# Optimization experiments

Hardware: AMD Instinct MI355X
Metric: run time of the kernel (lower is better)

The kernel has to match this reference:

```python
import jax, jax.numpy as jnp
import numpy as np

S, B, D_DEC, D_ALIGN, D_ENC = 1024, 64, 1024, 1024, 1024


def setup_inputs() -> dict:
    key = jax.random.key(0)
    ks = jax.random.split(key, 6)
    scale = 1.0 / np.sqrt(D_DEC)
    return {
        "s_tm1": jax.random.normal(ks[0], (B, D_DEC), jnp.float32),
        "xs_h": jax.random.normal(ks[1], (S, B, D_ENC), jnp.float32),
        "uh": jax.random.normal(ks[2], (S, B, D_ALIGN), jnp.float32),
        "xs_mask": jnp.ones((S, B), jnp.float32),
        "sa_w": jax.random.normal(ks[3], (D_ALIGN, D_DEC), jnp.float32) * scale,
        "sa_b": jnp.zeros((D_ALIGN,), jnp.float32),
        "a1_w": jax.random.normal(ks[4], (1, D_ALIGN), jnp.float32) * scale,
        "a1_b": jnp.zeros((1,), jnp.float32),
    }


def reference(s_tm1, xs_h, uh, xs_mask, sa_w, sa_b, a1_w, a1_b):
    # sa(s_tm1): [B, align]
    sa_s = s_tm1 @ sa_w.T + sa_b
    # broadcast-add over seq dim, tanh, then a1 (align -> 1), squeeze -> [S, B]
    h = jnp.tanh(sa_s[None, :, :] + uh)                  # [S, B, align]
    e = jnp.einsum('sba,a->sb', h, a1_w[0]) + a1_b[0]    # [S, B]
    # masked softmax over dim 0 (seq)
    ex = jnp.exp(e - jnp.max(e, axis=0, keepdims=True))
    ex = ex * xs_mask
    e_ij = ex / jnp.sum(ex, axis=0, keepdims=True)       # [S, B]
    # weighted sum over seq: [B, D_enc]
    attend = jnp.einsum('sb,sbd->bd', e_ij, xs_h)
    return (e_ij, attend)
```

## Files before the change

kernel.cpp:

```cpp
#include <hip/hip_runtime.h>
#include <hip/hip_bf16.h>

#define S_DIM 1024
#define B_DIM 64
#define A_DIM 1024

#define K2_CONST 2.8853900817779268f

#define K_TILE 64
#define KSPLIT 16
#define A_TILE 64
#define SSPLIT 32
#define S_CHUNK 32

typedef float f4 __attribute__((ext_vector_type(4)));

__device__ __forceinline__ float fast_exp2(float x) { return __builtin_amdgcn_exp2f(x); }
__device__ __forceinline__ float fast_rcp(float x)  { return __builtin_amdgcn_rcpf(x); }

__global__ __launch_bounds__(256) void gemm_partial_kernel(
    const float* __restrict__ s_tm1,
    const float* __restrict__ sa_w,
    float* __restrict__ part)
{
    __shared__ float sW[K_TILE][68];
    __shared__ float sS[K_TILE][68];
    const int a0 = blockIdx.x * A_TILE;
    const int k0 = blockIdx.y * K_TILE;
    const int t  = threadIdx.x;

    #pragma unroll
    for (int i = 0; i < 4; ++i) {
        int idx = t + 256 * i;
        int row = idx >> 4;
        int c4  = (idx & 15) * 4;
        f4 v = __builtin_nontemporal_load((const f4*)(sa_w + (size_t)(a0 + row) * 1024 + k0 + c4));
        sW[c4 + 0][row] = v.x; sW[c4 + 1][row] = v.y;
        sW[c4 + 2][row] = v.z; sW[c4 + 3][row] = v.w;
        f4 u = *(const f4*)(s_tm1 + (size_t)row * 1024 + k0 + c4);
        sS[c4 + 0][row] = u.x; sS[c4 + 1][row] = u.y;
        sS[c4 + 2][row] = u.z; sS[c4 + 3][row] = u.w;
    }
    __syncthreads();

    const int ta = (t & 15) * 4;
    const int tb = (t >> 4) * 4;
    float acc[4][4] = {};
    #pragma unroll 8
    for (int k = 0; k < K_TILE; ++k) {
        f4 wa = *(const f4*)&sW[k][ta];
        f4 sb = *(const f4*)&sS[k][tb];
        float wv[4] = {wa.x, wa.y, wa.z, wa.w};
        float sv[4] = {sb.x, sb.y, sb.z, sb.w};
        #pragma unroll
        for (int i = 0; i < 4; ++i)
            #pragma unroll
            for (int j = 0; j < 4; ++j)
                acc[i][j] = fmaf(wv[i], sv[j], acc[i][j]);
    }

    float* outp = part + (size_t)blockIdx.y * (B_DIM * 1024);
    #pragma unroll
    for (int j = 0; j < 4; ++j) {
        f4 v = {acc[0][j], acc[1][j], acc[2][j], acc[3][j]};
        *(f4*)(outp + (size_t)(tb + j) * 1024 + a0 + ta) = v;
    }
}

__global__ __launch_bounds__(256) void gemm_reduce_kernel(
    const float* __restrict__ part, const float* __restrict__ sa_b,
    float* __restrict__ ksa)
{
    int idx = blockIdx.x * 256 + threadIdx.x;
    int a = idx & 1023;
    float s = sa_b[a];
    #pragma unroll
    for (int kz = 0; kz < KSPLIT; ++kz)
        s += part[(size_t)kz * 65536 + idx];
    ksa[idx] = K2_CONST * s;
}

__global__ __launch_bounds__(256) void fused_kernel(
    const float* __restrict__ uh,
    const float* __restrict__ xs_h,
    const float* __restrict__ ksa,
    const float* __restrict__ a1_w,
    const float* __restrict__ xs_mask,
    float* __restrict__ ex_buf,
    float* __restrict__ psum,
    float* __restrict__ part)
{
    const int b    = blockIdx.x;
    const int sz   = blockIdx.y;
    const int s0   = sz * S_CHUNK;
    const int t    = threadIdx.x;
    const int lane = t & 63;
    const int w    = t >> 6;

    __shared__ float s_ex[S_CHUNK];
    __shared__ float s_mask[S_CHUNK];
    __shared__ f4 s_red[4][256];

    if (t < S_CHUNK) s_mask[t] = xs_mask[(size_t)(s0 + t) * B_DIM + b];

    const f4* sap = (const f4*)(ksa + (size_t)b * 1024);
    const f4* awp = (const f4*)a1_w;
    f4 sv[4], aw[4];
    #pragma unroll
    for (int j = 0; j < 4; ++j) { sv[j] = sap[lane + 64 * j]; aw[j] = awp[lane + 64 * j]; }

    __syncthreads();

    f4 acc4[4];
    #pragma unroll
    for (int j = 0; j < 4; ++j) { acc4[j].x = 0.f; acc4[j].y = 0.f; acc4[j].z = 0.f; acc4[j].w = 0.f; }

    #pragma unroll 2
    for (int k = 0; k < S_CHUNK / 4; ++k) {
        const int i = w + 4 * k;
        const size_t rowoff = ((size_t)(s0 + i) * B_DIM + b) * 1024;
        const f4* uhp = (const f4*)(uh + rowoff);
        const f4* xsp = (const f4*)(xs_h + rowoff);

        f4 xv[4];
        #pragma unroll
        for (int j = 0; j < 4; ++j) xv[j] = xsp[lane + 64 * j];

        float acc = 0.f;
        #pragma unroll
        for (int j = 0; j < 4; ++j) {
            f4 u = __builtin_nontemporal_load(&uhp[lane + 64 * j]);
            float t0 = fast_exp2(fmaf(K2_CONST, u.x, sv[j].x));
            float t1 = fast_exp2(fmaf(K2_CONST, u.y, sv[j].y));
            float t2 = fast_exp2(fmaf(K2_CONST, u.z, sv[j].z));
            float t3 = fast_exp2(fmaf(K2_CONST, u.w, sv[j].w));
            acc = fmaf(aw[j].x, fast_rcp(1.0f + t0), acc);
            acc = fmaf(aw[j].y, fast_rcp(1.0f + t1), acc);
            acc = fmaf(aw[j].z, fast_rcp(1.0f + t2), acc);
            acc = fmaf(aw[j].w, fast_rcp(1.0f + t3), acc);
        }
        #pragma unroll
        for (int off = 32; off; off >>= 1) acc += __shfl_xor(acc, off);

        float ex = fast_exp2(-K2_CONST * acc) * s_mask[i];
        if (lane == 0) s_ex[i] = ex;

        #pragma unroll
        for (int j = 0; j < 4; ++j) {
            acc4[j].x = fmaf(ex, xv[j].x, acc4[j].x);
            acc4[j].y = fmaf(ex, xv[j].y, acc4[j].y);
            acc4[j].z = fmaf(ex, xv[j].z, acc4[j].z);
            acc4[j].w = fmaf(ex, xv[j].w, acc4[j].w);
        }
    }

    #pragma unroll
    for (int j = 0; j < 4; ++j) s_red[w][lane + 64 * j] = acc4[j];
    __syncthreads();

    f4 r = s_red[0][t];
    #pragma unroll
    for (int ww = 1; ww < 4; ++ww) {
        f4 q = s_red[ww][t];
        r.x += q.x; r.y += q.y; r.z += q.z; r.w += q.w;
    }
    ((f4*)part)[((size_t)sz * B_DIM + b) * 256 + t] = r;

    if (t < S_CHUNK)
        ex_buf[(size_t)(s0 + t) * B_DIM + b] = s_ex[t];

    if (w == 0) {
        float v = (lane < S_CHUNK) ? s_ex[lane] : 0.f;
        #pragma unroll
        for (int off = 32; off; off >>= 1) v += __shfl_xor(v, off);
        if (lane == 0) psum[sz * B_DIM + b] = v;
    }
}

__global__ __launch_bounds__(256) void finalize_kernel(
    const float* __restrict__ ex_buf, const float* __restrict__ part,
    const float* __restrict__ psum,
    float* __restrict__ eij_out, float* __restrict__ att_out)
{
    const int blk = blockIdx.x;
    const int t = threadIdx.x;
    if (blk < 256) {
        int idx = blk * 256 + t;
        int b = idx & 63;
        float ssum = 0.f;
        #pragma unroll
        for (int sz = 0; sz < SSPLIT; ++sz) ssum += psum[sz * B_DIM + b];
        eij_out[idx] = ex_buf[idx] * (1.0f / ssum);
    } else {
        int idx = (blk - 256) * 256 + t;
        int b = idx >> 10;
        float ssum = 0.f;
        #pragma unroll
        for (int sz = 0; sz < SSPLIT; ++sz) ssum += psum[sz * B_DIM + b];
        float acc = 0.f;
        #pragma unroll
        for (int sz = 0; sz < SSPLIT; ++sz) acc += part[(size_t)sz * 65536 + idx];
        att_out[idx] = acc * (1.0f / ssum);
    }
}

extern "C" void kernel_launch(void* const* d_in, const int* in_sizes, int n_in,
                              void* d_out, int out_size, void* d_ws, size_t ws_size,
                              hipStream_t stream) {
    const float* s_tm1   = (const float*)d_in[0];
    const float* xs_h    = (const float*)d_in[1];
    const float* uh      = (const float*)d_in[2];
    const float* xs_mask = (const float*)d_in[3];
    const float* sa_w    = (const float*)d_in[4];
    const float* sa_b    = (const float*)d_in[5];
    const float* a1_w    = (const float*)d_in[6];

    float* eij_out = (float*)d_out;
    float* att_out = (float*)d_out + S_DIM * B_DIM;

    float* part_gemm = (float*)d_ws;
    float* ksa       = part_gemm + (size_t)KSPLIT * B_DIM * 1024;
    float* ex_buf    = ksa + 65536;
    float* part_att  = ex_buf + 65536;
    float* psum      = part_att + (size_t)SSPLIT * B_DIM * 1024;

    gemm_partial_kernel<<<dim3(A_DIM / A_TILE, KSPLIT), 256, 0, stream>>>(s_tm1, sa_w, part_gemm);
    gemm_reduce_kernel<<<65536 / 256, 256, 0, stream>>>(part_gemm, sa_b, ksa);
    fused_kernel<<<dim3(B_DIM, SSPLIT), 256, 0, stream>>>(uh, xs_h, ksa, a1_w, xs_mask,
                                                          ex_buf, psum, part_att);
    finalize_kernel<<<512, 256, 0, stream>>>(ex_buf, part_att, psum, eij_out, att_out);
}
```

Measured before the change: 105.0 us.

## Double-buffer uh/xs_h rows into LDS via async global_load_lds, enlarge sequence chunks

```diff
diff --git a/kernel.cpp b/kernel.cpp
--- a/kernel.cpp
+++ b/kernel.cpp
@@ -10,8 +10,9 @@
 #define K_TILE 64
 #define KSPLIT 16
 #define A_TILE 64
-#define SSPLIT 32
-#define S_CHUNK 32
+#define SSPLIT 8
+#define S_CHUNK 128
+#define NIT (S_CHUNK / 4)
 
 typedef float f4 __attribute__((ext_vector_type(4)));
 
@@ -80,6 +81,17 @@
     ksa[idx] = K2_CONST * s;
 }
 
+template <int AUX>
+__device__ __forceinline__ void stage_row(const float* g, float* lds_base, int lane) {
+    #pragma unroll
+    for (int j = 0; j < 4; ++j) {
+        __builtin_amdgcn_global_load_lds(
+            (const void*)(g + lane * 4 + j * 256),
+            (void*)((char*)lds_base + j * 1024),
+            16, 0, AUX);
+    }
+}
+
 __global__ __launch_bounds__(256) void fused_kernel(
     const float* __restrict__ uh,
     const float* __restrict__ xs_h,
@@ -97,9 +109,9 @@
     const int lane = t & 63;
     const int w    = t >> 6;
 
+    __shared__ float s_stage[4][4][1024];
     __shared__ float s_ex[S_CHUNK];
     __shared__ float s_mask[S_CHUNK];
-    __shared__ f4 s_red[4][256];
 
     if (t < S_CHUNK) s_mask[t] = xs_mask[(size_t)(s0 + t) * B_DIM + b];
 
@@ -115,25 +127,39 @@
     #pragma unroll
     for (int j = 0; j < 4; ++j) { acc4[j].x = 0.f; acc4[j].y = 0.f; acc4[j].z = 0.f; acc4[j].w = 0.f; }
 
-    #pragma unroll 2
-    for (int k = 0; k < S_CHUNK / 4; ++k) {
-        const int i = w + 4 * k;
-        const size_t rowoff = ((size_t)(s0 + i) * B_DIM + b) * 1024;
-        const f4* uhp = (const f4*)(uh + rowoff);
-        const f4* xsp = (const f4*)(xs_h + rowoff);
-
-        f4 xv[4];
-        #pragma unroll
-        for (int j = 0; j < 4; ++j) xv[j] = xsp[lane + 64 * j];
+    {
+        const size_t ro = ((size_t)(s0 + w) * B_DIM + b) * 1024;
+        stage_row<2>(uh + ro,   &s_stage[w][0][0], lane);
+        stage_row<0>(xs_h + ro, &s_stage[w][2][0], lane);
+    }
+
+    #pragma unroll 1
+    for (int k = 0; k < NIT; ++k) {
+        const int cur = k & 1;
+        const int nxt = cur ^ 1;
+        const int i   = w + 4 * k;
+
+        const int kn = (k < NIT - 1) ? (k + 1) : (NIT - 1);
+        const size_t rn = ((size_t)(s0 + w + 4 * kn) * B_DIM + b) * 1024;
+        stage_row<2>(uh + rn,   &s_stage[w][nxt][0], lane);
+        stage_row<0>(xs_h + rn, &s_stage[w][2 + nxt][0], lane);
+
+        asm volatile("s_waitcnt vmcnt(8)" ::: "memory");
+        __builtin_amdgcn_sched_barrier(0);
+
+        const f4* ub = (const f4*)&s_stage[w][cur][0];
+        const f4* xb = (const f4*)&s_stage[w][2 + cur][0];
+        f4 u[4], x[4];
+        #pragma unroll
+        for (int j = 0; j < 4; ++j) { u[j] = ub[lane + 64 * j]; x[j] = xb[lane + 64 * j]; }
 
         float acc = 0.f;
         #pragma unroll
         for (int j = 0; j < 4; ++j) {
-            f4 u = __builtin_nontemporal_load(&uhp[lane + 64 * j]);
-            float t0 = fast_exp2(fmaf(K2_CONST, u.x, sv[j].x));
-            float t1 = fast_exp2(fmaf(K2_CONST, u.y, sv[j].y));
-            float t2 = fast_exp2(fmaf(K2_CONST, u.z, sv[j].z));
-            float t3 = fast_exp2(fmaf(K2_CONST, u.w, sv[j].w));
+            float t0 = fast_exp2(fmaf(K2_CONST, u[j].x, sv[j].x));
+            float t1 = fast_exp2(fmaf(K2_CONST, u[j].y, sv[j].y));
+            float t2 = fast_exp2(fmaf(K2_CONST, u[j].z, sv[j].z));
+            float t3 = fast_exp2(fmaf(K2_CONST, u[j].w, sv[j].w));
             acc = fmaf(aw[j].x, fast_rcp(1.0f + t0), acc);
             acc = fmaf(aw[j].y, fast_rcp(1.0f + t1), acc);
             acc = fmaf(aw[j].z, fast_rcp(1.0f + t2), acc);
@@ -147,21 +173,25 @@
 
         #pragma unroll
         for (int j = 0; j < 4; ++j) {
-            acc4[j].x = fmaf(ex, xv[j].x, acc4[j].x);
-            acc4[j].y = fmaf(ex, xv[j].y, acc4[j].y);
-            acc4[j].z = fmaf(ex, xv[j].z, acc4[j].z);
-            acc4[j].w = fmaf(ex, xv[j].w, acc4[j].w);
+            acc4[j].x = fmaf(ex, x[j].x, acc4[j].x);
+            acc4[j].y = fmaf(ex, x[j].y, acc4[j].y);
+            acc4[j].z = fmaf(ex, x[j].z, acc4[j].z);
+            acc4[j].w = fmaf(ex, x[j].w, acc4[j].w);
         }
     }
 
-    #pragma unroll
-    for (int j = 0; j < 4; ++j) s_red[w][lane + 64 * j] = acc4[j];
+    asm volatile("s_waitcnt vmcnt(0)" ::: "memory");
+    __builtin_amdgcn_sched_barrier(0);
+
+    f4* red = (f4*)&s_stage[w][0][0];
+    #pragma unroll
+    for (int j = 0; j < 4; ++j) red[lane + 64 * j] = acc4[j];
     __syncthreads();
 
-    f4 r = s_red[0][t];
+    f4 r = ((const f4*)&s_stage[0][0][0])[t];
     #pragma unroll
     for (int ww = 1; ww < 4; ++ww) {
-        f4 q = s_red[ww][t];
+        f4 q = ((const f4*)&s_stage[ww][0][0])[t];
         r.x += q.x; r.y += q.y; r.z += q.z; r.w += q.w;
     }
     ((f4*)part)[((size_t)sz * B_DIM + b) * 256 + t] = r;
@@ -170,7 +200,7 @@
         ex_buf[(size_t)(s0 + t) * B_DIM + b] = s_ex[t];
 
     if (w == 0) {
-        float v = (lane < S_CHUNK) ? s_ex[lane] : 0.f;
+        float v = s_ex[lane] + s_ex[lane + 64];
         #pragma unroll
         for (int off = 32; off; off >>= 1) v += __shfl_xor(v, off);
         if (lane == 0) psum[sz * B_DIM + b] = v;
```

New measurement: 101.3 us. 1.04x faster.
